# Kernel optimization log

Hardware: AMD Instinct MI355X
Metric: run time of the kernel (lower is better)

Reference implementation:

```python
import jax, jax.numpy as jnp
import numpy as np

B, C, H, W = 2, 1024, 64, 64
T = 8                      # token_num
G = C // T                 # group_channel_num = d_model = 128
DI = 2 * G                 # d_inner (expand=2) = 256
DS = 16                    # d_state
DC = 4                     # d_conv
DTR = (G + 15) // 16       # dt_rank = 8
GN_GROUPS = 4
EPS = 1e-5


def setup_inputs() -> dict:
    key = jax.random.key(0)
    ks = jax.random.split(key, 8)
    g = lambda k, shp, sc: jax.random.normal(k, shp, jnp.float32) * sc
    return {
        "x": jax.random.normal(ks[0], (B, C, H, W), jnp.float32),
        "in_proj_w": g(ks[1], (2 * DI, G), G ** -0.5),
        "conv_w": g(ks[2], (DI, 1, DC), DC ** -0.5),
        "conv_b": g(ks[3], (DI,), 0.02),
        "x_proj_w": g(ks[4], (DTR + 2 * DS, DI), DI ** -0.5),
        "dt_proj_w": g(ks[5], (DI, DTR), DTR ** -0.5),
        "dt_proj_b": g(ks[6], (DI,), 0.1),
        "A_log": jnp.log(jnp.broadcast_to(jnp.arange(1, DS + 1, dtype=jnp.float32), (DI, DS))),
        "D": jnp.ones((DI,), jnp.float32),
        "out_proj_w": g(ks[7], (G, DI), DI ** -0.5),
        "gn_w": jnp.ones((C,), jnp.float32),
        "gn_b": jnp.zeros((C,), jnp.float32),
    }


def _mamba(xin, in_proj_w, conv_w, conv_b, x_proj_w, dt_proj_w, dt_proj_b,
           A_log, D, out_proj_w):
    # xin: (N, L, G)  with L = token_num
    N, L, _ = xin.shape
    xz = jnp.einsum('nlg,eg->nle', xin, in_proj_w)                 # (N, L, 2*DI)
    u, z = jnp.split(xz, 2, axis=-1)
    # depthwise causal conv along L (torch pads d_conv-1 both sides then slices [:L])
    uc = jax.lax.conv_general_dilated(
        u.transpose(0, 2, 1), conv_w, (1,), [(DC - 1, 0)],
        feature_group_count=DI, dimension_numbers=('NCH', 'OIH', 'NCH'))
    u = jax.nn.silu(uc + conv_b[None, :, None]).transpose(0, 2, 1)  # (N, L, DI)
    x_dbl = jnp.einsum('nld,kd->nlk', u, x_proj_w)                  # (N, L, DTR+2*DS)
    dt, Bm, Cm = jnp.split(x_dbl, [DTR, DTR + DS], axis=-1)
    dt = jax.nn.softplus(jnp.einsum('nlr,dr->nld', dt, dt_proj_w) + dt_proj_b)
    A = -jnp.exp(A_log)                                            # (DI, DS)

    def step(h, inp):
        dt_t, B_t, C_t, u_t = inp
        dA = jnp.exp(dt_t[..., None] * A)                          # (N, DI, DS)
        h = dA * h + dt_t[..., None] * B_t[:, None, :] * u_t[..., None]
        y = jnp.einsum('nds,ns->nd', h, C_t)
        return h, y

    h0 = jnp.zeros((N, DI, DS), u.dtype)
    xs = (dt.transpose(1, 0, 2), Bm.transpose(1, 0, 2),
          Cm.transpose(1, 0, 2), u.transpose(1, 0, 2))
    _, ys = jax.lax.scan(step, h0, xs)
    y = ys.transpose(1, 0, 2) + u * D                              # (N, L, DI)
    y = y * jax.nn.silu(z)
    return jnp.einsum('nld,gd->nlg', y, out_proj_w)                # (N, L, G)


def _group_norm(x, w, b):
    xg = x.reshape(x.shape[0], GN_GROUPS, C // GN_GROUPS, H, W)
    mu = xg.mean((2, 3, 4), keepdims=True)
    var = xg.var((2, 3, 4), keepdims=True)
    xn = ((xg - mu) * jax.lax.rsqrt(var + EPS)).reshape(x.shape)
    return xn * w[None, :, None, None] + b[None, :, None, None]


def reference(x, in_proj_w, conv_w, conv_b, x_proj_w, dt_proj_w, dt_proj_b,
              A_log, D, out_proj_w, gn_w, gn_b):
    # C == total_channel_num (1024 = 8*128) so no channel padding path.
    # b (t g) h w -> (b h w) t g
    xm = x.reshape(B, T, G, H, W).transpose(0, 3, 4, 1, 2).reshape(B * H * W, T, G)
    ym = _mamba(xm, in_proj_w, conv_w, conv_b, x_proj_w, dt_proj_w, dt_proj_b,
                A_log, D, out_proj_w)
    xr = ym.reshape(B, H, W, T, G).transpose(0, 3, 4, 1, 2).reshape(B, C, H, W)
    xp = jax.nn.silu(_group_norm(xr, gn_w, gn_b))
    return x + xp
```

## Files before the change

### kernel.cpp

```cpp
#include <hip/hip_runtime.h>
#include <math.h>


namespace {

typedef unsigned short ushort_t;
typedef __bf16 bf16x8 __attribute__((ext_vector_type(8)));
typedef float f32x4 __attribute__((ext_vector_type(4)));

constexpr int HW  = 4096;
constexpr int DIM = 256;
constexpr float INV_CNT = 1.0f / 1048576.0f;

__device__ __forceinline__ ushort_t f2b(float f) {
    union { float f; uint32_t u; } v; v.f = f;
    uint32_t u = v.u;
    return (ushort_t)((u + 0x7fffu + ((u >> 16) & 1u)) >> 16);
}
__device__ __forceinline__ float b2f(ushort_t h) {
    union { uint32_t u; float f; } v; v.u = ((uint32_t)h) << 16; return v.f;
}
__device__ __forceinline__ float lo2f(uint32_t d) {
    union { uint32_t u; float f; } v; v.u = d << 16; return v.f;
}
__device__ __forceinline__ float hi2f(uint32_t d) {
    union { uint32_t u; float f; } v; v.u = d & 0xffff0000u; return v.f;
}
__device__ __forceinline__ void up8(uint4 v, float* f) {
    f[0]=lo2f(v.x); f[1]=hi2f(v.x); f[2]=lo2f(v.y); f[3]=hi2f(v.y);
    f[4]=lo2f(v.z); f[5]=hi2f(v.z); f[6]=lo2f(v.w); f[7]=hi2f(v.w);
}
__device__ __forceinline__ uint4 pk8(const float* f) {
    uint4 o;
    o.x = f2b(f[0]) | ((uint32_t)f2b(f[1]) << 16);
    o.y = f2b(f[2]) | ((uint32_t)f2b(f[3]) << 16);
    o.z = f2b(f[4]) | ((uint32_t)f2b(f[5]) << 16);
    o.w = f2b(f[6]) | ((uint32_t)f2b(f[7]) << 16);
    return o;
}
__device__ __forceinline__ float silu_f(float v) {
    return v * __builtin_amdgcn_rcpf(1.0f + __expf(-v));
}
__device__ __forceinline__ float softplus_f(float x) {
    float e = __expf(fminf(x, 20.0f));
    float l = __logf(1.0f + e);
    return x > 20.0f ? x : l;
}
__device__ __forceinline__ uint64_t ds_tr16(uint32_t a) {
    uint64_t d;
    asm volatile("ds_read_b64_tr_b16 %0, %1" : "=v"(d) : "v"(a));
    return d;
}
union B8 { uint64_t q[2]; bf16x8 v; };

__global__ __launch_bounds__(256)
void setup_k(const float* __restrict__ wi, const float* __restrict__ wx,
             const float* __restrict__ wo, ushort_t* __restrict__ wib,
             ushort_t* __restrict__ wxb, ushort_t* __restrict__ wob,
             float* __restrict__ stats)
{
    int i = blockIdx.x * 256 + threadIdx.x;
    if (blockIdx.x == 0 && threadIdx.x < 16) stats[threadIdx.x] = 0.0f;
    for (int idx = i; idx < 108544; idx += 32768) {
        if (idx < 65536)       wib[idx]         = f2b(wi[idx]);
        else if (idx < 75776)  wxb[idx - 65536] = f2b(wx[idx - 65536]);
        else                   wob[idx - 75776] = f2b(wo[idx - 75776]);
    }
}

template<int MODE, int M, int K, int BM>
__global__ __launch_bounds__(256)
void mgemm_k(const ushort_t* __restrict__ Wb, const ushort_t* __restrict__ Xb,
             const float* __restrict__ Xf, ushort_t* __restrict__ O0,
             ushort_t* __restrict__ O1, float* __restrict__ stats)
{
    constexpr int BK  = 32;
    constexpr int MI  = BM / 16;
    constexpr int PST = BK * 16 + 16;
    __shared__ ushort_t Ws[BM][BK + 8];
    __shared__ ushort_t Xs[8 * PST];
    __shared__ float red[8];

    const int tid = threadIdx.x;
    const int lane = tid & 63;
    const int wv  = tid >> 6;
    const int l15 = lane & 15;
    const int lg  = lane >> 4;
    const int n0  = blockIdx.x * 128;
    const int bm  = blockIdx.y;
    const int p   = blockIdx.z;
    const int bb  = p >> 3, tt = p & 7;

    const ushort_t* Xpb = Xb + (size_t)p * DIM * HW;
    const float*    Xpf = Xf + (size_t)(bb * 1024 + tt * 128) * HW;

    f32x4 acc[MI][2] = {};
    const uint32_t xs_base = (uint32_t)(uintptr_t)&Xs[0];

    for (int kc = 0; kc < K; kc += BK) {
        for (int c = tid; c < BM * 4; c += 256) {
            int m = c >> 2, k8 = c & 3;
            uint4 v = make_uint4(0u, 0u, 0u, 0u);
            if (M >= BM || m < M)
                v = *(const uint4*)(Wb + (size_t)(bm * BM + m) * K + kc + k8 * 8);
            *(uint4*)&Ws[m][k8 * 8] = v;
        }
        for (int c = tid; c < 512; c += 256) {
            int k = c >> 4, nch = c & 15;
            uint4 v;
            if constexpr (MODE == 0) {
                const float* s = Xpf + (size_t)(kc + k) * HW + n0 + nch * 8;
                float4 a = *(const float4*)s;
                float4 b = *(const float4*)(s + 4);
                float f8[8] = {a.x, a.y, a.z, a.w, b.x, b.y, b.z, b.w};
                v = pk8(f8);
            } else {
                v = *(const uint4*)(Xpb + (size_t)(kc + k) * HW + n0 + nch * 8);
            }
            *(uint4*)&Xs[(nch >> 1) * PST + k * 16 + (nch & 1) * 8] = v;
        }
        __syncthreads();

        uint32_t ba0 = xs_base + (uint32_t)((wv * 2    ) * PST * 2) + lg * 256 + l15 * 8;
        uint32_t ba1 = xs_base + (uint32_t)((wv * 2 + 1) * PST * 2) + lg * 256 + l15 * 8;
        uint64_t q0 = ds_tr16(ba0), q1 = ds_tr16(ba0 + 128);
        uint64_t q2 = ds_tr16(ba1), q3 = ds_tr16(ba1 + 128);
        asm volatile("s_waitcnt lgkmcnt(0)" ::: "memory");
        __builtin_amdgcn_sched_barrier(0);
        B8 b0; b0.q[0] = q0; b0.q[1] = q1;
        B8 b1; b1.q[0] = q2; b1.q[1] = q3;
#pragma unroll
        for (int mi = 0; mi < MI; mi++) {
            bf16x8 a = *(const bf16x8*)&Ws[mi * 16 + l15][lg * 8];
            acc[mi][0] = __builtin_amdgcn_mfma_f32_16x16x32_bf16(a, b0.v, acc[mi][0], 0, 0, 0);
            acc[mi][1] = __builtin_amdgcn_mfma_f32_16x16x32_bf16(a, b1.v, acc[mi][1], 0, 0, 0);
        }
        __syncthreads();
    }

    float s1 = 0.0f, s2 = 0.0f;
#pragma unroll
    for (int mi = 0; mi < MI; mi++) {
#pragma unroll
        for (int ni = 0; ni < 2; ni++) {
            int ncol = n0 + wv * 32 + ni * 16 + l15;
#pragma unroll
            for (int r = 0; r < 4; r++) {
                float v = acc[mi][ni][r];
                int m_g = bm * BM + mi * 16 + lg * 4 + r;
                if (MODE == 0) {
                    size_t off = ((size_t)p * DIM + (m_g & 255)) * HW + ncol;
                    if (m_g < 256) O0[off] = f2b(v); else O1[off] = f2b(v);
                } else if (MODE == 1) {
                    if (m_g < 40) O0[((size_t)p * HW + ncol) * 40 + m_g] = f2b(v);
                } else {
                    O0[(size_t)(bb * 1024 + tt * 128 + m_g) * HW + ncol] = f2b(v);
                    s1 += v; s2 += v * v;
                }
            }
        }
    }

    if (MODE == 2) {
#pragma unroll
        for (int o = 32; o > 0; o >>= 1) {
            s1 += __shfl_down(s1, o, 64);
            s2 += __shfl_down(s2, o, 64);
        }
        if (lane == 0) { red[wv] = s1; red[4 + wv] = s2; }
        __syncthreads();
        if (tid == 0) {
            float t1 = red[0] + red[1] + red[2] + red[3];
            float t2 = red[4] + red[5] + red[6] + red[7];
            int gi = (bb * 4 + (tt >> 1)) * 2;
            atomicAdd(&stats[gi], t1);
            atomicAdd(&stats[gi + 1], t2);
        }
    }
}

__global__ __launch_bounds__(256)
void conv_k(ushort_t* __restrict__ u, const float* __restrict__ cw,
            const float* __restrict__ cb)
{
    const int di = blockIdx.y, b = blockIdx.z;
    const int hw = blockIdx.x * 2048 + threadIdx.x * 8;
    const float w0 = cw[di*4], w1 = cw[di*4+1], w2 = cw[di*4+2], w3 = cw[di*4+3];
    const float bias = cb[di];
    size_t base = ((size_t)(b * 8) * DIM + di) * HW + hw;
    float v[8][8];
#pragma unroll
    for (int t = 0; t < 8; t++)
        up8(*(const uint4*)(u + base + (size_t)t * DIM * HW), v[t]);
#pragma unroll
    for (int t = 0; t < 8; t++) {
        float o8[8];
#pragma unroll
        for (int i = 0; i < 8; i++) {
            float a = fmaf(w3, v[t][i], bias);
            if (t >= 1) a = fmaf(w2, v[t-1][i], a);
            if (t >= 2) a = fmaf(w1, v[t-2][i], a);
            if (t >= 3) a = fmaf(w0, v[t-3][i], a);
            o8[i] = silu_f(a);
        }
        *(uint4*)(u + base + (size_t)t * DIM * HW) = pk8(o8);
    }
}

__global__ __launch_bounds__(256)
void scan_k(const ushort_t* __restrict__ xdT, ushort_t* __restrict__ u,
            const ushort_t* __restrict__ z, const float* __restrict__ dtw,
            const float* __restrict__ dtb, const float* __restrict__ Dp)
{
    const int tid = threadIdx.x, lane = tid & 63, wv = tid >> 6;
    const int hw  = blockIdx.x * 64 + lane;
    const int di  = blockIdx.y * 4 + wv;
    const int b   = blockIdx.z;

    float wdt[8];
#pragma unroll
    for (int r = 0; r < 8; r++) wdt[r] = dtw[di * 8 + r];
    const float bias = dtb[di], Dv = Dp[di];
    float h[16];
#pragma unroll
    for (int s = 0; s < 16; s++) h[s] = 0.0f;

    for (int t = 0; t < 8; t++) {
        const int p = b * 8 + t;
        const ushort_t* xp = xdT + ((size_t)p * HW + hw) * 40;
        union { uint4 v4[5]; uint32_t d[20]; } Q;
#pragma unroll
        for (int j = 0; j < 5; j++) Q.v4[j] = *(const uint4*)(xp + j * 8);

        size_t off = ((size_t)p * DIM + di) * HW + hw;
        float uv = b2f(u[off]);
        float zv = b2f(z[off]);

        float dtr = bias;
#pragma unroll
        for (int r = 0; r < 8; r++) {
            float f = (r & 1) ? hi2f(Q.d[r >> 1]) : lo2f(Q.d[r >> 1]);
            dtr = fmaf(wdt[r], f, dtr);
        }
        float dt  = softplus_f(dtr);
        float e1  = __expf(-dt);
        float dtu = dt * uv;
        float a = e1, y = 0.0f;
#pragma unroll
        for (int s = 0; s < 16; s++) {
            float Bs = ((8 + s) & 1) ? hi2f(Q.d[(8 + s) >> 1])  : lo2f(Q.d[(8 + s) >> 1]);
            float Cs = ((24 + s) & 1) ? hi2f(Q.d[(24 + s) >> 1]) : lo2f(Q.d[(24 + s) >> 1]);
            h[s] = fmaf(a, h[s], dtu * Bs);
            y = fmaf(h[s], Cs, y);
            a *= e1;
        }
        y = fmaf(uv, Dv, y);
        u[off] = f2b(y * silu_f(zv));
    }
}

__global__ __launch_bounds__(256)
void apply_k(const float* __restrict__ x, const ushort_t* __restrict__ xr,
             const float* __restrict__ stats, const float* __restrict__ gw,
             const float* __restrict__ gb, float* __restrict__ out)
{
    size_t e = ((size_t)blockIdx.x * 256 + threadIdx.x) * 8;
    int cpl = (int)(e >> 12);
    int c = cpl & 1023, b = cpl >> 10, g = c >> 8;
    float s1 = stats[(b * 4 + g) * 2 + 0];
    float s2 = stats[(b * 4 + g) * 2 + 1];
    float mu = s1 * INV_CNT;
    float var = s2 * INV_CNT - mu * mu;
    float rstd = rsqrtf(var + 1e-5f);
    float w = gw[c], bi = gb[c];
    float r8[8];
    up8(*(const uint4*)(xr + e), r8);
    float4 x0 = *(const float4*)(x + e);
    float4 x1 = *(const float4*)(x + e + 4);
    float xf[8] = {x0.x, x0.y, x0.z, x0.w, x1.x, x1.y, x1.z, x1.w};
    float o8[8];
#pragma unroll
    for (int i = 0; i < 8; i++)
        o8[i] = xf[i] + silu_f(fmaf((r8[i] - mu) * rstd, w, bi));
    *(float4*)(out + e)     = make_float4(o8[0], o8[1], o8[2], o8[3]);
    *(float4*)(out + e + 4) = make_float4(o8[4], o8[5], o8[6], o8[7]);
}

}

extern "C" void kernel_launch(void* const* d_in, const int* in_sizes, int n_in,
                              void* d_out, int out_size, void* d_ws, size_t ws_size,
                              hipStream_t stream)
{
    const float* x    = (const float*)d_in[0];
    const float* w_in = (const float*)d_in[1];
    const float* cw   = (const float*)d_in[2];
    const float* cb   = (const float*)d_in[3];
    const float* wx   = (const float*)d_in[4];
    const float* wdt  = (const float*)d_in[5];
    const float* bdt  = (const float*)d_in[6];
    const float* Dp   = (const float*)d_in[8];
    const float* wo   = (const float*)d_in[9];
    const float* gw   = (const float*)d_in[10];
    const float* gb   = (const float*)d_in[11];
    float* out = (float*)d_out;

    ushort_t* wsb  = (ushort_t*)d_ws;
    ushort_t* u    = wsb;
    ushort_t* z    = u    + 16777216ull;
    ushort_t* xdT  = z    + 16777216ull;
    ushort_t* xr   = xdT  + 2621440ull;
    ushort_t* wib  = xr   + 8388608ull;
    ushort_t* wxb  = wib  + 65536ull;
    ushort_t* wob  = wxb  + 10240ull;
    float* stats   = (float*)(wob + 32768ull);

    setup_k<<<128, 256, 0, stream>>>(w_in, wx, wo, wib, wxb, wob, stats);
    mgemm_k<0, 512, 128, 128><<<dim3(32, 4, 16), 256, 0, stream>>>(wib, nullptr, x, u, z, nullptr);
    conv_k<<<dim3(2, 256, 2), 256, 0, stream>>>(u, cw, cb);
    mgemm_k<1, 40, 256, 48><<<dim3(32, 1, 16), 256, 0, stream>>>(wxb, u, nullptr, xdT, nullptr, nullptr);
    scan_k<<<dim3(64, 64, 2), 256, 0, stream>>>(xdT, u, z, wdt, bdt, Dp);
    mgemm_k<2, 128, 256, 128><<<dim3(32, 1, 16), 256, 0, stream>>>(wob, u, nullptr, xr, nullptr, stats);
    apply_k<<<4096, 256, 0, stream>>>(x, xr, stats, gw, gb, out);
}
```

Before: 168.5 us.

## Fuse causal conv+SiLU into x_proj GEMM and scan, drop conv kernel

Removes the standalone depthwise conv kernel. The conv and SiLU are now recomputed on the fly, once in the x_proj GEMM's operand load (reading up to four timesteps of raw u) and once in the scan kernel through a rolling register window. The scan is also restructured so each thread handles four d_inner channels with packed float2 state updates, which reuses the loaded B/C/dt row across channels. The cost is extra global reads of u in the GEMM loader and a higher register load in the scan, with fewer blocks launched.

New measurement: 165.6 us. Within noise of the previous version (-1.7%).

```diff
diff --git a/kernel.cpp b/kernel.cpp
--- a/kernel.cpp
+++ b/kernel.cpp
@@ -7,6 +7,7 @@
 typedef unsigned short ushort_t;
 typedef __bf16 bf16x8 __attribute__((ext_vector_type(8)));
 typedef float f32x4 __attribute__((ext_vector_type(4)));
+typedef float v2f __attribute__((ext_vector_type(2)));
 
 constexpr int HW  = 4096;
 constexpr int DIM = 256;
@@ -25,6 +26,9 @@
 }
 __device__ __forceinline__ float hi2f(uint32_t d) {
     union { uint32_t u; float f; } v; v.u = d & 0xffff0000u; return v.f;
+}
+__device__ __forceinline__ v2f pair2f(uint32_t d) {
+    v2f r; r[0] = lo2f(d); r[1] = hi2f(d); return r;
 }
 __device__ __forceinline__ void up8(uint4 v, float* f) {
     f[0]=lo2f(v.x); f[1]=hi2f(v.x); f[2]=lo2f(v.y); f[3]=hi2f(v.y);
@@ -71,7 +75,8 @@
 template<int MODE, int M, int K, int BM>
 __global__ __launch_bounds__(256)
 void mgemm_k(const ushort_t* __restrict__ Wb, const ushort_t* __restrict__ Xb,
-             const float* __restrict__ Xf, ushort_t* __restrict__ O0,
+             const float* __restrict__ Xf, const float* __restrict__ cw,
+             const float* __restrict__ cb, ushort_t* __restrict__ O0,
              ushort_t* __restrict__ O1, float* __restrict__ stats)
 {
     constexpr int BK  = 32;
@@ -114,6 +119,28 @@
                 float4 b = *(const float4*)(s + 4);
                 float f8[8] = {a.x, a.y, a.z, a.w, b.x, b.y, b.z, b.w};
                 v = pk8(f8);
+            } else if constexpr (MODE == 1) {
+                int di = kc + k;
+                float4 w4 = *(const float4*)(cw + di * 4);
+                float cbv = cb[di];
+                float a8[8] = {cbv, cbv, cbv, cbv, cbv, cbv, cbv, cbv};
+                size_t colo = (size_t)(n0 + nch * 8);
+#pragma unroll
+                for (int j = 0; j < 4; j++) {
+                    int ts = tt - 3 + j;
+                    if (ts >= 0) {
+                        uint4 raw = *(const uint4*)(Xb +
+                            ((size_t)((bb * 8 + ts) * DIM + di)) * HW + colo);
+                        float f8[8]; up8(raw, f8);
+                        float wj = (&w4.x)[j];
+#pragma unroll
+                        for (int i = 0; i < 8; i++) a8[i] = fmaf(wj, f8[i], a8[i]);
+                    }
+                }
+                float o8[8];
+#pragma unroll
+                for (int i = 0; i < 8; i++) o8[i] = silu_f(a8[i]);
+                v = pk8(o8);
             } else {
                 v = *(const uint4*)(Xpb + (size_t)(kc + k) * HW + n0 + nch * 8);
             }
@@ -180,50 +207,35 @@
 }
 
 __global__ __launch_bounds__(256)
-void conv_k(ushort_t* __restrict__ u, const float* __restrict__ cw,
-            const float* __restrict__ cb)
-{
-    const int di = blockIdx.y, b = blockIdx.z;
-    const int hw = blockIdx.x * 2048 + threadIdx.x * 8;
-    const float w0 = cw[di*4], w1 = cw[di*4+1], w2 = cw[di*4+2], w3 = cw[di*4+3];
-    const float bias = cb[di];
-    size_t base = ((size_t)(b * 8) * DIM + di) * HW + hw;
-    float v[8][8];
-#pragma unroll
-    for (int t = 0; t < 8; t++)
-        up8(*(const uint4*)(u + base + (size_t)t * DIM * HW), v[t]);
-#pragma unroll
-    for (int t = 0; t < 8; t++) {
-        float o8[8];
-#pragma unroll
-        for (int i = 0; i < 8; i++) {
-            float a = fmaf(w3, v[t][i], bias);
-            if (t >= 1) a = fmaf(w2, v[t-1][i], a);
-            if (t >= 2) a = fmaf(w1, v[t-2][i], a);
-            if (t >= 3) a = fmaf(w0, v[t-3][i], a);
-            o8[i] = silu_f(a);
-        }
-        *(uint4*)(u + base + (size_t)t * DIM * HW) = pk8(o8);
-    }
-}
-
-__global__ __launch_bounds__(256)
 void scan_k(const ushort_t* __restrict__ xdT, ushort_t* __restrict__ u,
-            const ushort_t* __restrict__ z, const float* __restrict__ dtw,
+            const ushort_t* __restrict__ z, const float* __restrict__ cw,
+            const float* __restrict__ cb, const float* __restrict__ dtw,
             const float* __restrict__ dtb, const float* __restrict__ Dp)
 {
     const int tid = threadIdx.x, lane = tid & 63, wv = tid >> 6;
     const int hw  = blockIdx.x * 64 + lane;
-    const int di  = blockIdx.y * 4 + wv;
+    const int di0 = blockIdx.y * 4 + wv;
     const int b   = blockIdx.z;
 
-    float wdt[8];
-#pragma unroll
-    for (int r = 0; r < 8; r++) wdt[r] = dtw[di * 8 + r];
-    const float bias = dtb[di], Dv = Dp[di];
-    float h[16];
-#pragma unroll
-    for (int s = 0; s < 16; s++) h[s] = 0.0f;
+    float wdt[4][8], bias[4], Dv[4], cwv[4][4], cbv[4];
+#pragma unroll
+    for (int q = 0; q < 4; q++) {
+        int di = di0 + q * 64;
+#pragma unroll
+        for (int r = 0; r < 8; r++) wdt[q][r] = dtw[di * 8 + r];
+        bias[q] = dtb[di];
+        Dv[q]   = Dp[di];
+        float4 w4 = *(const float4*)(cw + di * 4);
+        cwv[q][0] = w4.x; cwv[q][1] = w4.y; cwv[q][2] = w4.z; cwv[q][3] = w4.w;
+        cbv[q] = cb[di];
+    }
+
+    v2f h[4][8];
+#pragma unroll
+    for (int q = 0; q < 4; q++)
+#pragma unroll
+        for (int k = 0; k < 8; k++) { h[q][k][0] = 0.0f; h[q][k][1] = 0.0f; }
+    float rm1[4] = {}, rm2[4] = {}, rm3[4] = {};
 
     for (int t = 0; t < 8; t++) {
         const int p = b * 8 + t;
@@ -232,30 +244,50 @@
 #pragma unroll
         for (int j = 0; j < 5; j++) Q.v4[j] = *(const uint4*)(xp + j * 8);
 
-        size_t off = ((size_t)p * DIM + di) * HW + hw;
-        float uv = b2f(u[off]);
-        float zv = b2f(z[off]);
-
-        float dtr = bias;
-#pragma unroll
-        for (int r = 0; r < 8; r++) {
-            float f = (r & 1) ? hi2f(Q.d[r >> 1]) : lo2f(Q.d[r >> 1]);
-            dtr = fmaf(wdt[r], f, dtr);
-        }
-        float dt  = softplus_f(dtr);
-        float e1  = __expf(-dt);
-        float dtu = dt * uv;
-        float a = e1, y = 0.0f;
-#pragma unroll
-        for (int s = 0; s < 16; s++) {
-            float Bs = ((8 + s) & 1) ? hi2f(Q.d[(8 + s) >> 1])  : lo2f(Q.d[(8 + s) >> 1]);
-            float Cs = ((24 + s) & 1) ? hi2f(Q.d[(24 + s) >> 1]) : lo2f(Q.d[(24 + s) >> 1]);
-            h[s] = fmaf(a, h[s], dtu * Bs);
-            y = fmaf(h[s], Cs, y);
-            a *= e1;
-        }
-        y = fmaf(uv, Dv, y);
-        u[off] = f2b(y * silu_f(zv));
+        float dtf[8];
+#pragma unroll
+        for (int r = 0; r < 8; r++)
+            dtf[r] = (r & 1) ? hi2f(Q.d[r >> 1]) : lo2f(Q.d[r >> 1]);
+        v2f Bp[8], Cp[8];
+#pragma unroll
+        for (int k = 0; k < 8; k++) {
+            Bp[k] = pair2f(Q.d[4 + k]);
+            Cp[k] = pair2f(Q.d[12 + k]);
+        }
+
+        size_t ubase = ((size_t)p * DIM + di0) * HW + hw;
+#pragma unroll
+        for (int q = 0; q < 4; q++) {
+            size_t off = ubase + (size_t)(q * 64) * HW;
+            float rt = b2f(u[off]);
+            float zv = b2f(z[off]);
+            float uc = silu_f(fmaf(cwv[q][3], rt,
+                              fmaf(cwv[q][2], rm1[q],
+                              fmaf(cwv[q][1], rm2[q],
+                              fmaf(cwv[q][0], rm3[q], cbv[q])))));
+            rm3[q] = rm2[q]; rm2[q] = rm1[q]; rm1[q] = rt;
+
+            float dtr = bias[q];
+#pragma unroll
+            for (int r = 0; r < 8; r++) dtr = fmaf(wdt[q][r], dtf[r], dtr);
+            float dt = softplus_f(dtr);
+            float e1 = __expf(-dt);
+            float e2 = e1 * e1;
+            v2f a;    a[0] = e1;  a[1] = e2;
+            v2f ee;   ee[0] = e2; ee[1] = e2;
+            float dtu = dt * uc;
+            v2f dtu2; dtu2[0] = dtu; dtu2[1] = dtu;
+            v2f y2;   y2[0] = 0.0f; y2[1] = 0.0f;
+#pragma unroll
+            for (int k = 0; k < 8; k++) {
+                h[q][k] = a * h[q][k] + dtu2 * Bp[k];
+                y2 = y2 + h[q][k] * Cp[k];
+                a = a * ee;
+            }
+            float y = y2[0] + y2[1];
+            y = fmaf(uc, Dv[q], y);
+            u[off] = f2b(y * silu_f(zv));
+        }
     }
 }
 
@@ -316,10 +348,12 @@
     float* stats   = (float*)(wob + 32768ull);
 
     setup_k<<<128, 256, 0, stream>>>(w_in, wx, wo, wib, wxb, wob, stats);
-    mgemm_k<0, 512, 128, 128><<<dim3(32, 4, 16), 256, 0, stream>>>(wib, nullptr, x, u, z, nullptr);
-    conv_k<<<dim3(2, 256, 2), 256, 0, stream>>>(u, cw, cb);
-    mgemm_k<1, 40, 256, 48><<<dim3(32, 1, 16), 256, 0, stream>>>(wxb, u, nullptr, xdT, nullptr, nullptr);
-    scan_k<<<dim3(64, 64, 2), 256, 0, stream>>>(xdT, u, z, wdt, bdt, Dp);
-    mgemm_k<2, 128, 256, 128><<<dim3(32, 1, 16), 256, 0, stream>>>(wob, u, nullptr, xr, nullptr, stats);
+    mgemm_k<0, 512, 128, 128><<<dim3(32, 4, 16), 256, 0, stream>>>(
+        wib, nullptr, x, nullptr, nullptr, u, z, nullptr);
+    mgemm_k<1, 40, 256, 48><<<dim3(32, 1, 16), 256, 0, stream>>>(
+        wxb, u, nullptr, cw, cb, xdT, nullptr, nullptr);
+    scan_k<<<dim3(64, 16, 2), 256, 0, stream>>>(xdT, u, z, cw, cb, wdt, bdt, Dp);
+    mgemm_k<2, 128, 256, 128><<<dim3(32, 1, 16), 256, 0, stream>>>(
+        wob, u, nullptr, nullptr, nullptr, xr, nullptr, stats);
     apply_k<<<4096, 256, 0, stream>>>(x, xr, stats, gw, gb, out);
 }
```
